# Optimization experiments

Hardware: AMD Instinct MI355X
Metric: run time of the kernel (lower is better)

Reference implementation:

```python
import jax, jax.numpy as jnp
import numpy as np

DIM = 1024
HEADS = 16


def setup_inputs() -> dict:
    key = jax.random.key(0)
    k1, k2, k3, k4 = jax.random.split(key, 4)
    x = jax.random.normal(k1, (4, 2048, DIM), dtype=jnp.float32)
    s = 1.0 / np.sqrt(DIM)
    w_qkv = jax.random.normal(k2, (DIM, 3 * DIM), dtype=jnp.float32) * s
    w_out = jax.random.normal(k3, (DIM, DIM), dtype=jnp.float32) * s
    b_out = jax.random.normal(k4, (DIM,), dtype=jnp.float32) * 0.01
    return {"x": x, "w_qkv": w_qkv, "w_out": w_out, "b_out": b_out}


def reference(x, w_qkv, w_out, b_out):
    b, n, d = x.shape
    h = HEADS
    dh = d // h
    scale = dh ** -0.5
    qkv = x @ w_qkv  # [b, n, 3d]
    q, k, v = jnp.split(qkv, 3, axis=-1)
    # [b, n, d] -> [b, h, n, dh]
    def to_heads(t):
        return t.reshape(b, n, h, dh).transpose(0, 2, 1, 3)
    q, k, v = to_heads(q), to_heads(k), to_heads(v)
    dots = jnp.einsum('bhid,bhjd->bhij', q, k) * scale
    attn = jax.nn.softmax(dots, axis=-1)
    out = jnp.einsum('bhij,bhjd->bhid', attn, v)
    out = out.transpose(0, 2, 1, 3).reshape(b, n, d)
    return out @ w_out + b_out
```

## Files before the change

### kernel.cpp

```cpp
#include <hip/hip_runtime.h>
#include <hip/hip_bf16.h>


typedef __attribute__((ext_vector_type(4))) float f32x4;
typedef __attribute__((ext_vector_type(16))) float f32x16;
typedef __attribute__((ext_vector_type(8))) unsigned short u16x8;
typedef __attribute__((ext_vector_type(4))) unsigned short u16x4;
typedef __attribute__((ext_vector_type(4))) unsigned int u32x4;
typedef __attribute__((ext_vector_type(8))) __bf16 bf16x8;

static __device__ __forceinline__ f32x4 mfma_bf16(u16x8 a, u16x8 b, f32x4 c) {
    return __builtin_amdgcn_mfma_f32_16x16x32_bf16(
        __builtin_bit_cast(bf16x8, a), __builtin_bit_cast(bf16x8, b), c, 0, 0, 0);
}
static __device__ __forceinline__ f32x16 mfma32(u16x8 a, u16x8 b, f32x16 c) {
    return __builtin_amdgcn_mfma_f32_32x32x16_bf16(
        __builtin_bit_cast(bf16x8, a), __builtin_bit_cast(bf16x8, b), c, 0, 0, 0);
}

static __device__ __forceinline__ unsigned short f2bf(float f) {
    unsigned int u = __builtin_bit_cast(unsigned int, f);
    u += 0x7fffu + ((u >> 16) & 1u);
    return (unsigned short)(u >> 16);
}
static __device__ __forceinline__ unsigned int cvt_pk_bf16(float a, float b) {
    unsigned int r;
    asm("v_cvt_pk_bf16_f32 %0, %1, %2" : "=v"(r) : "v"(a), "v"(b));
    return r;
}
static __device__ __forceinline__ float fexp2(float x) {
    float r;
    asm("v_exp_f32 %0, %1" : "=v"(r) : "v"(x));
    return r;
}
static __device__ __forceinline__ float frcp(float x) {
    float r;
    asm("v_rcp_f32 %0, %1" : "=v"(r) : "v"(x));
    return r;
}
typedef const __attribute__((address_space(1))) unsigned int* gp1_t;
typedef __attribute__((address_space(3))) unsigned int* lp3_t;
static __device__ __forceinline__ void gl_lds16(const void* g, void* l) {
    __builtin_amdgcn_global_load_lds((gp1_t)g, (lp3_t)l, 16, 0, 0);
}

__global__ void k_cvt(const float* __restrict__ in, unsigned short* __restrict__ out, int n4) {
    int i = blockIdx.x * blockDim.x + threadIdx.x;
    int stride = gridDim.x * blockDim.x;
    for (; i < n4; i += stride) {
        f32x4 v = ((const f32x4*)in)[i];
        u16x4 o;
        #pragma unroll
        for (int j = 0; j < 4; ++j) o[j] = f2bf(v[j]);
        ((u16x4*)out)[i] = o;
    }
}

__global__ void k_transpose_sc(const float* __restrict__ in, unsigned short* __restrict__ out,
                               int R, int C, int scale_rows, float scale) {
    __shared__ float tile[32][33];
    int c0 = blockIdx.x * 32, r0 = blockIdx.y * 32;
    int tx = threadIdx.x, ty = threadIdx.y;
    #pragma unroll
    for (int i = ty; i < 32; i += 8)
        tile[i][tx] = in[(size_t)(r0 + i) * C + c0 + tx];
    __syncthreads();
    #pragma unroll
    for (int i = ty; i < 32; i += 8) {
        float v = tile[tx][i];
        if (c0 + i < scale_rows) v *= scale;
        out[(size_t)(c0 + i) * R + r0 + tx] = f2bf(v);
    }
}

__global__ __launch_bounds__(512, 1) void k_gemm1p(
    const unsigned short* __restrict__ A,
    const unsigned short* __restrict__ BT,
    unsigned short* __restrict__ qkv)
{
    __shared__ unsigned short As[3][256 * 64];
    __shared__ unsigned short Bs[3][128 * 64];
    const int K = 1024;
    const int tid = threadIdx.x, lane = tid & 63, wave = tid >> 6;

    int lin = blockIdx.y * 8 + blockIdx.x;
    int virt = (lin & 7) * 32 + (lin >> 3);
    int bxg = virt % 8, by = virt / 8;
    const int m0 = by * 256;

    const int wm = (wave >> 1) * 64, wn = (wave & 1) * 64;
    const int lr = lane & 15, half = lane >> 4;
    const int srow = lane >> 3, sslot = lane & 7;

    auto stage_sub = [&](int buf, int g, int h) {
        int k0 = (g & 15) * 64;
        int n0 = ((g >> 4) * 8 + bxg) * 128;
        #pragma unroll
        for (int r = 0; r < 2; ++r) {
            int chunk = (h * 2 + r) * 8 + wave;
            int row = chunk * 8 + srow;
            int koff = (sslot ^ (row & 7)) * 8;
            gl_lds16(&A[(size_t)(m0 + row) * K + k0 + koff], &As[buf][chunk * 512]);
        }
        {
            int chunk = h * 8 + wave;
            int row = chunk * 8 + srow;
            int koff = (sslot ^ (row & 7)) * 8;
            gl_lds16(&BT[(size_t)(n0 + row) * K + k0 + koff], &Bs[buf][chunk * 512]);
        }
    };

    f32x4 acc[4][4] = {};

    stage_sub(0, 0, 0); stage_sub(0, 0, 1);
    stage_sub(1, 1, 0); stage_sub(1, 1, 1);
    asm volatile("s_waitcnt vmcnt(6)" ::: "memory");
    __builtin_amdgcn_s_barrier();

    for (int t = 0; t < 48; ++t) {
        const int cur = t % 3, nxt = (t + 2) % 3;
        const bool do_stage = (t + 2) < 48;
        const unsigned short* Ab = As[cur];
        const unsigned short* Bb = Bs[cur];

        #pragma unroll
        for (int ks = 0; ks < 2; ++ks) {
            u16x8 af[4], bfr[4];
            #pragma unroll
            for (int i = 0; i < 4; ++i) {
                int ra = wm + i * 16 + lr;
                af[i] = *(const u16x8*)&Ab[ra * 64 + (((ks * 4 + half) ^ (ra & 7)) * 8)];
                int rb = wn + i * 16 + lr;
                bfr[i] = *(const u16x8*)&Bb[rb * 64 + (((ks * 4 + half) ^ (rb & 7)) * 8)];
            }
            if (do_stage) stage_sub(nxt, t + 2, ks);
            if (ks == 1) {
                if (t < 46)       asm volatile("s_waitcnt vmcnt(6)" ::: "memory");
                else if (t == 46) asm volatile("s_waitcnt vmcnt(0)" ::: "memory");
            }
            __builtin_amdgcn_s_barrier();
            asm volatile("s_waitcnt lgkmcnt(0)" ::: "memory");
            __builtin_amdgcn_sched_barrier(0);
            __builtin_amdgcn_s_setprio(1);
            #pragma unroll
            for (int i = 0; i < 4; ++i)
                #pragma unroll
                for (int j = 0; j < 4; ++j)
                    acc[i][j] = mfma_bf16(af[i], bfr[j], acc[i][j]);
            __builtin_amdgcn_s_setprio(0);
            __builtin_amdgcn_s_barrier();
        }

        if ((t & 15) == 15) {
            int n0 = ((t >> 4) * 8 + bxg) * 128;
            #pragma unroll
            for (int i = 0; i < 4; ++i)
                #pragma unroll
                for (int j = 0; j < 4; ++j) {
                    #pragma unroll
                    for (int r = 0; r < 4; ++r) {
                        int row = m0 + wm + i * 16 + half * 4 + r;
                        int col = n0 + wn + j * 16 + lr;
                        qkv[(size_t)row * 3072 + col] = f2bf(acc[i][j][r]);
                    }
                    acc[i][j] = f32x4{0.f, 0.f, 0.f, 0.f};
                }
        }
    }
}

__global__ void k_vtrans(const unsigned short* __restrict__ qkv,
                         unsigned short* __restrict__ VTs) {
    __shared__ unsigned short tile[32][33];
    int bh = blockIdx.y >> 1, dt = blockIdx.y & 1;
    int b = bh >> 4, h = bh & 15;
    int n0 = blockIdx.x * 32, d0 = dt * 32;
    int tx = threadIdx.x, ty = threadIdx.y;
    const unsigned short* src = qkv + (size_t)(b * 2048) * 3072 + 2048 + h * 64 + d0;
    #pragma unroll
    for (int i = ty; i < 32; i += 8)
        tile[i][tx] = src[(size_t)(n0 + i) * 3072 + tx];
    __syncthreads();
    #pragma unroll
    for (int i = ty; i < 32; i += 8)
        VTs[((size_t)bh * 64 + d0 + i) * 2048 + n0 + tx] = tile[tx][i];
}

__global__ __launch_bounds__(512, 1) void k_gemm2(
    const unsigned short* __restrict__ A,
    const unsigned short* __restrict__ BT,
    const float* __restrict__ bias,
    float* __restrict__ outf)
{
    __shared__ unsigned short As[3][256 * 64];
    __shared__ unsigned short Bs[3][128 * 64];
    const int K = 1024;
    const int tid = threadIdx.x, lane = tid & 63, wave = tid >> 6;

    int lin = blockIdx.y * 8 + blockIdx.x;
    int virt = (lin & 7) * 32 + (lin >> 3);
    int bx = virt % 8, by = virt / 8;
    const int m0 = by * 256, n0 = bx * 128;

    const int wm = (wave >> 1) * 64, wn = (wave & 1) * 64;
    const int lr = lane & 15, half = lane >> 4;
    const int srow = lane >> 3, sslot = lane & 7;

    auto stage_sub = [&](int buf, int t, int h) {
        int k0 = t * 64;
        #pragma unroll
        for (int r = 0; r < 2; ++r) {
            int chunk = (h * 2 + r) * 8 + wave;
            int row = chunk * 8 + srow;
            int koff = (sslot ^ (row & 7)) * 8;
            gl_lds16(&A[(size_t)(m0 + row) * K + k0 + koff], &As[buf][chunk * 512]);
        }
        {
            int chunk = h * 8 + wave;
            int row = chunk * 8 + srow;
            int koff = (sslot ^ (row & 7)) * 8;
            gl_lds16(&BT[(size_t)(n0 + row) * K + k0 + koff], &Bs[buf][chunk * 512]);
        }
    };

    f32x4 acc[4][4] = {};

    stage_sub(0, 0, 0); stage_sub(0, 0, 1);
    stage_sub(1, 1, 0); stage_sub(1, 1, 1);
    asm volatile("s_waitcnt vmcnt(6)" ::: "memory");
    __builtin_amdgcn_s_barrier();

    for (int t = 0; t < 16; ++t) {
        const int cur = t % 3, nxt = (t + 2) % 3;
        const bool do_stage = (t + 2) < 16;
        const unsigned short* Ab = As[cur];
        const unsigned short* Bb = Bs[cur];

        #pragma unroll
        for (int ks = 0; ks < 2; ++ks) {
            u16x8 af[4], bfr[4];
            #pragma unroll
            for (int i = 0; i < 4; ++i) {
                int ra = wm + i * 16 + lr;
                af[i] = *(const u16x8*)&Ab[ra * 64 + (((ks * 4 + half) ^ (ra & 7)) * 8)];
                int rb = wn + i * 16 + lr;
                bfr[i] = *(const u16x8*)&Bb[rb * 64 + (((ks * 4 + half) ^ (rb & 7)) * 8)];
            }
            if (do_stage) stage_sub(nxt, t + 2, ks);
            if (ks == 1) {
                if (t < 14)       asm volatile("s_waitcnt vmcnt(6)" ::: "memory");
                else if (t == 14) asm volatile("s_waitcnt vmcnt(0)" ::: "memory");
            }
            __builtin_amdgcn_s_barrier();
            asm volatile("s_waitcnt lgkmcnt(0)" ::: "memory");
            __builtin_amdgcn_sched_barrier(0);
            __builtin_amdgcn_s_setprio(1);
            #pragma unroll
            for (int i = 0; i < 4; ++i)
                #pragma unroll
                for (int j = 0; j < 4; ++j)
                    acc[i][j] = mfma_bf16(af[i], bfr[j], acc[i][j]);
            __builtin_amdgcn_s_setprio(0);
            __builtin_amdgcn_s_barrier();
        }
    }

    #pragma unroll
    for (int i = 0; i < 4; ++i)
        #pragma unroll
        for (int j = 0; j < 4; ++j)
            #pragma unroll
            for (int r = 0; r < 4; ++r) {
                int row = m0 + wm + i * 16 + half * 4 + r;
                int col = n0 + wn + j * 16 + lr;
                outf[(size_t)row * 1024 + col] = acc[i][j][r] + bias[col];
            }
}

__global__ __launch_bounds__(256, 4) void k_attn(
    const unsigned short* __restrict__ qkv,
    const unsigned short* __restrict__ VTs,
    unsigned short* __restrict__ attn)
{
    __shared__ unsigned short Kt[2][64 * 64];
    __shared__ unsigned short Vt[2][64 * 64];
    const int tid = threadIdx.x, lane = tid & 63, wave = tid >> 6;

    int lin = blockIdx.y * 16 + blockIdx.x;
    int virt = (lin & 7) * 128 + (lin >> 3);
    int bh = virt >> 4;
    int q0 = (virt & 15) * 128 + wave * 32;

    const int lq = lane & 31;
    const int hi = lane >> 5;

    int b = bh >> 4, h = bh & 15;
    const unsigned short* Kq = qkv + (size_t)(b * 2048) * 3072 + 1024 + h * 64;
    const unsigned short* Vbase = VTs + (size_t)bh * 64 * 2048;

    u16x8 qf[4];
    {
        const unsigned short* Qr = qkv + (size_t)(b * 2048 + q0 + lq) * 3072 + h * 64;
        #pragma unroll
        for (int kk = 0; kk < 4; ++kk)
            qf[kk] = *(const u16x8*)&Qr[kk * 16 + hi * 8];
    }

    const int srow_in = lane >> 4, sslot = lane & 15;
    auto stage = [&](int buf, int j0) {
        #pragma unroll
        for (int c = 0; c < 2; ++c) {
            int chunk = wave * 2 + c;
            int row = chunk * 4 + srow_in;
            int v = sslot ^ (row & 15);
            int high = v >> 3, dsl = (v & 7) * 8;
            gl_lds16(Kq + (size_t)(j0 + high * 32 + row) * 3072 + dsl, &Kt[buf][chunk * 512]);
            gl_lds16(Vbase + (size_t)(high * 32 + row) * 2048 + j0 + dsl, &Vt[buf][chunk * 512]);
        }
    };

    f32x16 o[2] = {};
    f32x16 osum = {};
    const u16x8 onesf = {0x3F80, 0x3F80, 0x3F80, 0x3F80, 0x3F80, 0x3F80, 0x3F80, 0x3F80};

    stage(0, 0);
    __syncthreads();
    int cur = 0;

    for (int t = 0; t < 32; ++t) {
        if (t < 31) stage(cur ^ 1, (t + 1) * 64);

        f32x16 sacc[2] = {};
        __builtin_amdgcn_s_setprio(1);
        #pragma unroll
        for (int jb = 0; jb < 2; ++jb) {
            u16x8 kf[4];
            #pragma unroll
            for (int kk = 0; kk < 4; ++kk) {
                int s = (jb * 8 + kk * 2 + hi) ^ (lq & 15);
                kf[kk] = *(const u16x8*)&Kt[cur][lq * 128 + s * 8];
            }
            #pragma unroll
            for (int kk = 0; kk < 4; ++kk)
                sacc[jb] = mfma32(kf[kk], qf[kk], sacc[jb]);
        }
        __builtin_amdgcn_s_setprio(0);

        unsigned int pk[16];
        #pragma unroll
        for (int jb = 0; jb < 2; ++jb)
            #pragma unroll
            for (int i = 0; i < 8; ++i)
                pk[jb * 8 + i] = cvt_pk_bf16(fexp2(sacc[jb][2 * i]), fexp2(sacc[jb][2 * i + 1]));

        __builtin_amdgcn_s_setprio(1);
        #pragma unroll
        for (int kk = 0; kk < 4; ++kk) {
            const int base = (kk >> 1) * 8 + (kk & 1) * 4;
            unsigned int w0 = pk[base + 0], w2 = pk[base + 2];
            unsigned int w1 = pk[base + 1], w3 = pk[base + 3];
            asm("v_permlane32_swap_b32 %0, %1" : "+v"(w0), "+v"(w2));
            asm("v_permlane32_swap_b32 %0, %1" : "+v"(w1), "+v"(w3));
            u32x4 w; w[0] = w0; w[1] = w1; w[2] = w2; w[3] = w3;
            u16x8 pa = __builtin_bit_cast(u16x8, w);
            osum = mfma32(pa, onesf, osum);
            #pragma unroll
            for (int db = 0; db < 2; ++db) {
                int s = (db * 8 + kk * 2 + hi) ^ (lq & 15);
                u16x8 vf = *(const u16x8*)&Vt[cur][lq * 128 + s * 8];
                o[db] = mfma32(pa, vf, o[db]);
            }
        }
        __builtin_amdgcn_s_setprio(0);

        __syncthreads();
        cur ^= 1;
    }

    #pragma unroll
    for (int r = 0; r < 16; ++r) {
        int qrow = (r & 3) + 8 * (r >> 2) + 4 * hi;
        float invr = frcp(osum[r]);
        size_t ro = (size_t)(b * 2048 + q0 + qrow) * 1024 + h * 64;
        attn[ro + lq]      = f2bf(o[0][r] * invr);
        attn[ro + 32 + lq] = f2bf(o[1][r] * invr);
    }
}

extern "C" void kernel_launch(void* const* d_in, const int* in_sizes, int n_in,
                              void* d_out, int out_size, void* d_ws, size_t ws_size,
                              hipStream_t stream) {
    const float* x     = (const float*)d_in[0];
    const float* w_qkv = (const float*)d_in[1];
    const float* w_out = (const float*)d_in[2];
    const float* b_out = (const float*)d_in[3];
    float* out = (float*)d_out;

    char* ws = (char*)d_ws;
    size_t off = 0;
    auto alloc = [&](size_t bytes) -> void* {
        void* p = ws + off;
        off += (bytes + 255) & ~(size_t)255;
        return p;
    };
    unsigned short* xb    = (unsigned short*)alloc(8192ull * 1024 * 2);
    unsigned short* wqkvT = (unsigned short*)alloc(3072ull * 1024 * 2);
    unsigned short* woutT = (unsigned short*)alloc(1024ull * 1024 * 2);
    unsigned short* qkv   = (unsigned short*)alloc(8192ull * 3072 * 2);
    unsigned short* VTs   = (unsigned short*)alloc(64ull * 2048 * 64 * 2);
    if (off > ws_size) return;

    k_cvt<<<2048, 256, 0, stream>>>(x, xb, 8192 * 1024 / 4);
    k_transpose_sc<<<dim3(3072 / 32, 1024 / 32), dim3(32, 8), 0, stream>>>(
        w_qkv, wqkvT, 1024, 3072, 1024, 0.18033688f);
    k_transpose_sc<<<dim3(1024 / 32, 1024 / 32), dim3(32, 8), 0, stream>>>(
        w_out, woutT, 1024, 1024, 0, 1.0f);
    k_gemm1p<<<dim3(8, 32), 512, 0, stream>>>(xb, wqkvT, qkv);
    k_vtrans<<<dim3(64, 128), dim3(32, 8), 0, stream>>>(qkv, VTs);
    k_attn<<<dim3(16, 64), 256, 0, stream>>>(qkv, VTs, xb);
    k_gemm2<<<dim3(8, 32), 512, 0, stream>>>(xb, woutT, b_out, out);
}
```

Before: 193.3 us.

## Widen QKV GEMM tile to 256x384 with double-buffered full-K loop

Replaces the persistent QKV projection kernel, which walked three 128-wide column tiles in sequence with a triple-buffered pipeline, with one 256x384 output tile per block over the full K. The tile loop is now 16 steps with double buffering and one barrier per step, and each wave holds 4x12 accumulators. Each B fragment is loaded from shared memory and used immediately across the four A fragments. The intent is more reuse of A per load and fewer barriers and epilogue phases. In exchange the kernel uses far more accumulator registers, a shallower prefetch pipeline and more shared memory.

```diff
diff --git a/kernel.cpp b/kernel.cpp
--- a/kernel.cpp
+++ b/kernel.cpp
@@ -73,100 +73,90 @@
     }
 }
 
-__global__ __launch_bounds__(512, 1) void k_gemm1p(
+__global__ __launch_bounds__(512, 1) void k_gemm1f(
     const unsigned short* __restrict__ A,
     const unsigned short* __restrict__ BT,
     unsigned short* __restrict__ qkv)
 {
-    __shared__ unsigned short As[3][256 * 64];
-    __shared__ unsigned short Bs[3][128 * 64];
+    __shared__ unsigned short As[2][256 * 64];
+    __shared__ unsigned short Bs[2][384 * 64];
     const int K = 1024;
     const int tid = threadIdx.x, lane = tid & 63, wave = tid >> 6;
 
     int lin = blockIdx.y * 8 + blockIdx.x;
-    int virt = (lin & 7) * 32 + (lin >> 3);
-    int bxg = virt % 8, by = virt / 8;
-    const int m0 = by * 256;
-
-    const int wm = (wave >> 1) * 64, wn = (wave & 1) * 64;
+    int xcd = lin & 7, idx = lin >> 3;
+    int by = xcd * 4 + (idx >> 3);
+    int bxg = idx & 7;
+    const int m0 = by * 256, n0 = bxg * 384;
+
+    const int wm = (wave >> 1) * 64, wn = (wave & 1) * 192;
     const int lr = lane & 15, half = lane >> 4;
     const int srow = lane >> 3, sslot = lane & 7;
 
-    auto stage_sub = [&](int buf, int g, int h) {
-        int k0 = (g & 15) * 64;
-        int n0 = ((g >> 4) * 8 + bxg) * 128;
-        #pragma unroll
-        for (int r = 0; r < 2; ++r) {
-            int chunk = (h * 2 + r) * 8 + wave;
+    auto stage = [&](int buf, int t) {
+        int k0 = t * 64;
+        #pragma unroll
+        for (int r = 0; r < 4; ++r) {
+            int chunk = r * 8 + wave;
             int row = chunk * 8 + srow;
             int koff = (sslot ^ (row & 7)) * 8;
             gl_lds16(&A[(size_t)(m0 + row) * K + k0 + koff], &As[buf][chunk * 512]);
         }
-        {
-            int chunk = h * 8 + wave;
+        #pragma unroll
+        for (int r = 0; r < 6; ++r) {
+            int chunk = r * 8 + wave;
             int row = chunk * 8 + srow;
             int koff = (sslot ^ (row & 7)) * 8;
             gl_lds16(&BT[(size_t)(n0 + row) * K + k0 + koff], &Bs[buf][chunk * 512]);
         }
     };
 
-    f32x4 acc[4][4] = {};
-
-    stage_sub(0, 0, 0); stage_sub(0, 0, 1);
-    stage_sub(1, 1, 0); stage_sub(1, 1, 1);
-    asm volatile("s_waitcnt vmcnt(6)" ::: "memory");
+    f32x4 acc[4][12] = {};
+
+    stage(0, 0);
+    asm volatile("s_waitcnt vmcnt(0)" ::: "memory");
     __builtin_amdgcn_s_barrier();
 
-    for (int t = 0; t < 48; ++t) {
-        const int cur = t % 3, nxt = (t + 2) % 3;
-        const bool do_stage = (t + 2) < 48;
+    for (int t = 0; t < 16; ++t) {
+        const int cur = t & 1;
+        if (t < 15) stage(cur ^ 1, t + 1);
         const unsigned short* Ab = As[cur];
         const unsigned short* Bb = Bs[cur];
 
         #pragma unroll
         for (int ks = 0; ks < 2; ++ks) {
-            u16x8 af[4], bfr[4];
+            u16x8 af[4];
             #pragma unroll
             for (int i = 0; i < 4; ++i) {
                 int ra = wm + i * 16 + lr;
                 af[i] = *(const u16x8*)&Ab[ra * 64 + (((ks * 4 + half) ^ (ra & 7)) * 8)];
-                int rb = wn + i * 16 + lr;
-                bfr[i] = *(const u16x8*)&Bb[rb * 64 + (((ks * 4 + half) ^ (rb & 7)) * 8)];
-            }
-            if (do_stage) stage_sub(nxt, t + 2, ks);
-            if (ks == 1) {
-                if (t < 46)       asm volatile("s_waitcnt vmcnt(6)" ::: "memory");
-                else if (t == 46) asm volatile("s_waitcnt vmcnt(0)" ::: "memory");
-            }
-            __builtin_amdgcn_s_barrier();
-            asm volatile("s_waitcnt lgkmcnt(0)" ::: "memory");
-            __builtin_amdgcn_sched_barrier(0);
-            __builtin_amdgcn_s_setprio(1);
-            #pragma unroll
-            for (int i = 0; i < 4; ++i)
+            }
+            #pragma unroll
+            for (int j = 0; j < 12; ++j) {
+                int rb = wn + j * 16 + lr;
+                u16x8 bfr = *(const u16x8*)&Bb[rb * 64 + (((ks * 4 + half) ^ (rb & 7)) * 8)];
+                __builtin_amdgcn_s_setprio(1);
                 #pragma unroll
-                for (int j = 0; j < 4; ++j)
-                    acc[i][j] = mfma_bf16(af[i], bfr[j], acc[i][j]);
-            __builtin_amdgcn_s_setprio(0);
-            __builtin_amdgcn_s_barrier();
-        }
-
-        if ((t & 15) == 15) {
-            int n0 = ((t >> 4) * 8 + bxg) * 128;
-            #pragma unroll
-            for (int i = 0; i < 4; ++i)
-                #pragma unroll
-                for (int j = 0; j < 4; ++j) {
-                    #pragma unroll
-                    for (int r = 0; r < 4; ++r) {
-                        int row = m0 + wm + i * 16 + half * 4 + r;
-                        int col = n0 + wn + j * 16 + lr;
-                        qkv[(size_t)row * 3072 + col] = f2bf(acc[i][j][r]);
-                    }
-                    acc[i][j] = f32x4{0.f, 0.f, 0.f, 0.f};
-                }
-        }
-    }
+                for (int i = 0; i < 4; ++i)
+                    acc[i][j] = mfma_bf16(af[i], bfr, acc[i][j]);
+                __builtin_amdgcn_s_setprio(0);
+            }
+        }
+
+        asm volatile("s_waitcnt vmcnt(0) lgkmcnt(0)" ::: "memory");
+        __builtin_amdgcn_s_barrier();
+    }
+
+    #pragma unroll
+    for (int i = 0; i < 4; ++i)
+        #pragma unroll
+        for (int j = 0; j < 12; ++j)
+            #pragma unroll
+            for (int r = 0; r < 4; ++r) {
+                int row = m0 + wm + i * 16 + half * 4 + r;
+                int col = n0 + wn + j * 16 + lr;
+                qkv[(size_t)row * 3072 + col] = f2bf(acc[i][j][r]);
+            }
 }
 
 __global__ void k_vtrans(const unsigned short* __restrict__ qkv,
@@ -415,7 +405,7 @@
         w_qkv, wqkvT, 1024, 3072, 1024, 0.18033688f);
     k_transpose_sc<<<dim3(1024 / 32, 1024 / 32), dim3(32, 8), 0, stream>>>(
         w_out, woutT, 1024, 1024, 0, 1.0f);
-    k_gemm1p<<<dim3(8, 32), 512, 0, stream>>>(xb, wqkvT, qkv);
+    k_gemm1f<<<dim3(8, 32), 512, 0, stream>>>(xb, wqkvT, qkv);
     k_vtrans<<<dim3(64, 128), dim3(32, 8), 0, stream>>>(qkv, VTs);
     k_attn<<<dim3(16, 64), 256, 0, stream>>>(qkv, VTs, xb);
     k_gemm2<<<dim3(8, 32), 512, 0, stream>>>(xb, woutT, b_out, out);
```

Measured after the change: 190.9 us. About the same (-1.2%).
